# Kernel tuning notes

Hardware: AMD Instinct MI355X
Metric: run time of the kernel (lower is better)

The kernel has to match this reference:

```python
import jax, jax.numpy as jnp
import numpy as np

D_MODEL = 1024
NUM_HEADS = 16
D_FF = 4096
BATCH = 4
SEQ = 1024
EPS = 1e-5
ROPE_THETA = 10000.0


def trunc_normal(key, shape):
    # approximate torch trunc_normal_(mean=0, std=1, a=-2, b=2)
    return jax.random.truncated_normal(key, -2.0, 2.0, shape, dtype=jnp.float32)


def setup_inputs() -> dict:
    key = jax.random.key(0)
    ks = jax.random.split(key, 10)
    d, h, f = D_MODEL, NUM_HEADS, D_FF
    return {
        "x": jax.random.normal(ks[0], (BATCH, SEQ, d), dtype=jnp.float32),
        "wq": trunc_normal(ks[1], (d, d)),
        "wk": trunc_normal(ks[2], (d, d)),
        "wv": trunc_normal(ks[3], (d, d)),
        "wo": trunc_normal(ks[4], (d, d)),
        "w1": trunc_normal(ks[5], (f, d)),
        "w2": trunc_normal(ks[6], (d, f)),
        "w3": trunc_normal(ks[7], (f, d)),
        "g1": trunc_normal(ks[8], (d,)),
        "g2": trunc_normal(ks[9], (d,)),
    }


def rms_norm(x, g):
    # source sums (x^2 + eps) then divides by d -> mean(x^2) + eps
    rms = jnp.sqrt(jnp.mean(jnp.square(x), axis=-1, keepdims=True) + EPS)
    return x * g / rms


def apply_rope(x, pos):
    # x: [b, h, s, d_k]; interleaved-pair rotation, theta=ROPE_THETA
    dk = x.shape[-1]
    inv_freq = ROPE_THETA ** (-jnp.arange(0, dk, 2, dtype=jnp.float32) / dk)
    ang = pos[:, None].astype(jnp.float32) * inv_freq[None, :]  # [s, dk/2]
    cos, sin = jnp.cos(ang), jnp.sin(ang)
    x1, x2 = x[..., 0::2], x[..., 1::2]
    r1 = x1 * cos - x2 * sin
    r2 = x1 * sin + x2 * cos
    return jnp.stack([r1, r2], axis=-1).reshape(x.shape)


def reference(x, wq, wk, wv, wo, w1, w2, w3, g1, g2):
    b, s, d = x.shape
    h, dk = NUM_HEADS, d // NUM_HEADS
    pos = jnp.arange(s)

    # --- attention sub-block (pre-norm) ---
    y = rms_norm(x, g1)
    q = (y @ wq.T).reshape(b, s, h, dk).transpose(0, 2, 1, 3)
    k = (y @ wk.T).reshape(b, s, h, dk).transpose(0, 2, 1, 3)
    v = (y @ wv.T).reshape(b, s, h, dk).transpose(0, 2, 1, 3)
    q = apply_rope(q, pos)
    k = apply_rope(k, pos)
    scores = jnp.einsum('bhqd,bhkd->bhqk', q, k) / jnp.sqrt(jnp.float32(dk))
    causal = jnp.tril(jnp.ones((s, s), dtype=bool))
    scores = jnp.where(causal, scores, -jnp.inf)
    attn = jax.nn.softmax(scores, axis=-1)
    ctx = jnp.einsum('bhqk,bhkd->bhqd', attn, v)
    ctx = ctx.transpose(0, 2, 1, 3).reshape(b, s, d)
    x = x + ctx @ wo.T

    # --- SwiGLU FFN sub-block (pre-norm) ---
    y = rms_norm(x, g2)
    l1 = y @ w1.T
    glu = (jax.nn.sigmoid(l1) * l1) * (y @ w3.T)
    return x + glu @ w2.T
```

## Files before the change

kernel.cpp:

```cpp
#include <hip/hip_runtime.h>

typedef __bf16 bf16;
typedef __attribute__((ext_vector_type(8))) __bf16 bf16x8;
typedef __attribute__((ext_vector_type(4))) float f32x4;

static __device__ __forceinline__ int swz4(int r) { return (r >> 1) & 3; }

static __device__ __forceinline__ void async_cp16(void* lds, const void* g) {
  __builtin_amdgcn_global_load_lds((__attribute__((address_space(1))) void*)g,
                                   (__attribute__((address_space(3))) void*)lds,
                                   16, 0, 0);
}

static __device__ __forceinline__ f32x4 mfma16(bf16x8 a, bf16x8 b, f32x4 c) {
  return __builtin_amdgcn_mfma_f32_16x16x32_bf16(a, b, c, 0, 0, 0);
}

static __device__ __forceinline__ unsigned short bfbits(float f) {
  bf16 b = (bf16)f;
  return __builtin_bit_cast(unsigned short, b);
}

extern "C" __global__ void prep_kernel(
    const float* __restrict__ wq, const float* __restrict__ wk,
    const float* __restrict__ wv, const float* __restrict__ wo,
    const float* __restrict__ w1, const float* __restrict__ w3,
    const float* __restrict__ w2,
    unsigned short* __restrict__ WQH, unsigned short* __restrict__ WQL,
    unsigned short* __restrict__ WKH, unsigned short* __restrict__ WKL,
    unsigned short* __restrict__ WVH, unsigned short* __restrict__ WOH,
    unsigned short* __restrict__ W1H, unsigned short* __restrict__ W3H,
    unsigned short* __restrict__ W2H, float2* __restrict__ rope) {
  const int seg = blockIdx.y;
  const int i = blockIdx.x * 256 + threadIdx.x;
  if (seg == 7) {
    if (i >= 32768) return;
    int s = i >> 5, fi = i & 31;
    float inv_freq = powf(10000.0f, -(2.0f * (float)fi) / 64.0f);
    float ang = (float)s * inv_freq;
    float2 cs;
    cs.x = cosf(ang);
    cs.y = sinf(ang);
    rope[i] = cs;
    return;
  }
  const float* src;
  unsigned short* hi_;
  unsigned short* lo_ = nullptr;
  int n4;
  switch (seg) {
    case 0: src = wq; hi_ = WQH; lo_ = WQL; n4 = 262144; break;
    case 1: src = wk; hi_ = WKH; lo_ = WKL; n4 = 262144; break;
    case 2: src = wv; hi_ = WVH; n4 = 262144; break;
    case 3: src = wo; hi_ = WOH; n4 = 262144; break;
    case 4: src = w1; hi_ = W1H; n4 = 1048576; break;
    case 5: src = w3; hi_ = W3H; n4 = 1048576; break;
    default: src = w2; hi_ = W2H; n4 = 1048576; break;
  }
  if (i >= n4) return;
  float4 v = ((const float4*)src)[i];
  bf16 b0 = (bf16)v.x, b1 = (bf16)v.y, b2 = (bf16)v.z, b3 = (bf16)v.w;
  ushort4 oh;
  oh.x = __builtin_bit_cast(unsigned short, b0);
  oh.y = __builtin_bit_cast(unsigned short, b1);
  oh.z = __builtin_bit_cast(unsigned short, b2);
  oh.w = __builtin_bit_cast(unsigned short, b3);
  ((ushort4*)hi_)[i] = oh;
  if (lo_) {
    ushort4 ol;
    ol.x = bfbits(v.x - (float)b0);
    ol.y = bfbits(v.y - (float)b1);
    ol.z = bfbits(v.z - (float)b2);
    ol.w = bfbits(v.w - (float)b3);
    ((ushort4*)lo_)[i] = ol;
  }
}

extern "C" __global__ __launch_bounds__(256) void rmsnorm_kernel(
    const float* __restrict__ x, const float* __restrict__ g,
    unsigned short* __restrict__ yhi, unsigned short* __restrict__ ylo) {
  int row = blockIdx.x;
  int t = threadIdx.x;
  const float4 xv = *(const float4*)(x + (size_t)row * 1024 + t * 4);
  float ss = xv.x * xv.x + xv.y * xv.y + xv.z * xv.z + xv.w * xv.w;
#pragma unroll
  for (int d = 1; d < 64; d <<= 1) ss += __shfl_xor(ss, d, 64);
  __shared__ float red[4];
  if ((t & 63) == 0) red[t >> 6] = ss;
  __syncthreads();
  float tot = red[0] + red[1] + red[2] + red[3];
  float inv = 1.0f / sqrtf(tot * (1.0f / 1024.0f) + 1e-5f);
  const float4 gv = *(const float4*)(g + t * 4);
  float y0 = xv.x * gv.x * inv, y1 = xv.y * gv.y * inv;
  float y2 = xv.z * gv.z * inv, y3 = xv.w * gv.w * inv;
  bf16 b0 = (bf16)y0, b1 = (bf16)y1, b2 = (bf16)y2, b3 = (bf16)y3;
  ushort4 oh;
  oh.x = __builtin_bit_cast(unsigned short, b0);
  oh.y = __builtin_bit_cast(unsigned short, b1);
  oh.z = __builtin_bit_cast(unsigned short, b2);
  oh.w = __builtin_bit_cast(unsigned short, b3);
  ((ushort4*)yhi)[(size_t)row * 256 + t] = oh;
  if (ylo) {
    ushort4 ol;
    ol.x = bfbits(y0 - (float)b0);
    ol.y = bfbits(y1 - (float)b1);
    ol.z = bfbits(y2 - (float)b2);
    ol.w = bfbits(y3 - (float)b3);
    ((ushort4*)ylo)[(size_t)row * 256 + t] = ol;
  }
}

template <int EPI>
__global__ __launch_bounds__(256, 2) void gemm_nt(
    const bf16* __restrict__ A, const bf16* __restrict__ B, int N, int K, int ldk,
    float* __restrict__ outF, bf16* __restrict__ outB,
    const float* __restrict__ resF) {
  const int bid = blockIdx.x;
  const int xcd = bid & 7, sq = bid >> 3;
  const int z = sq >> 5;
  const int rem = sq & 31;
  const size_t tm = (size_t)(xcd * 4 + (rem >> 3)) * 128;
  const size_t tn = (size_t)(rem & 7) * 128;
  A += (size_t)z * K;
  B += (size_t)z * K;
  __shared__ alignas(16) bf16 As[128 * 32];
  __shared__ alignas(16) bf16 Bs[128 * 32];
  const int tid = threadIdx.x;
  const int lane = tid & 63, wave = tid >> 6;
  const int lo = lane & 15, hi = lane >> 4;
  const int wm = wave >> 1, wn = wave & 1;
  f32x4 acc[4][4] = {};
  for (int k0 = 0; k0 < K; k0 += 32) {
    __syncthreads();
#pragma unroll
    for (int i2 = 0; i2 < 2; i2++) {
      int p = tid + 256 * i2;
      int row = p >> 2, kcp = p & 3;
      int kcl = kcp ^ swz4(row);
      async_cp16((char*)As + (size_t)p * 16, A + (tm + row) * (size_t)ldk + k0 + kcl * 8);
      async_cp16((char*)Bs + (size_t)p * 16, B + (tn + row) * (size_t)ldk + k0 + kcl * 8);
    }
    __syncthreads();
    bf16x8 fa[4], fb[4];
#pragma unroll
    for (int i = 0; i < 4; i++) {
      int ra = wm * 64 + i * 16 + lo;
      fa[i] = *(const bf16x8*)((const char*)As + ra * 64 + ((hi ^ swz4(ra)) << 4));
      int rb = wn * 64 + i * 16 + lo;
      fb[i] = *(const bf16x8*)((const char*)Bs + rb * 64 + ((hi ^ swz4(rb)) << 4));
    }
    __builtin_amdgcn_s_setprio(1);
#pragma unroll
    for (int i = 0; i < 4; i++)
#pragma unroll
      for (int j = 0; j < 4; j++) acc[i][j] = mfma16(fa[i], fb[j], acc[i][j]);
    __builtin_amdgcn_s_setprio(0);
  }
#pragma unroll
  for (int i = 0; i < 4; i++)
#pragma unroll
    for (int j = 0; j < 4; j++)
#pragma unroll
      for (int r = 0; r < 4; r++) {
        size_t m = tm + wm * 64 + i * 16 + hi * 4 + r;
        size_t n = tn + wn * 64 + j * 16 + lo;
        float v = acc[i][j][r];
        if constexpr (EPI == 0) {
          size_t idx = (((m >> 10) * 16 + (n >> 6)) * 64 + (n & 63)) * 1024 + (m & 1023);
          outB[idx] = (bf16)v;
        } else if constexpr (EPI == 1) {
          size_t idx = m * (size_t)N + n;
          outF[idx] = v + resF[idx];
        } else {
          atomicAdd(&outF[m * (size_t)N + n], v);
        }
      }
}

extern "C" __global__ __launch_bounds__(512, 2) void gemm_up_kernel(
    const bf16* __restrict__ A, const bf16* __restrict__ B1,
    const bf16* __restrict__ B3, bf16* __restrict__ G) {
  __shared__ alignas(16) bf16 LA[2][2][256][32];
  __shared__ alignas(16) bf16 LB1[2][2][128][32];
  __shared__ alignas(16) bf16 LB3[2][2][128][32];
  const int tid = threadIdx.x;
  const int lane = tid & 63, wave = tid >> 6;
  const int lo = lane & 15, hi = lane >> 4;
  const int wm = wave >> 1, wn = wave & 1;
  const int bid = blockIdx.x;
  const int xcd = bid & 7, sq = bid >> 3;
  const size_t tn = (size_t)(xcd * 4 + (sq & 3)) * 128;
  const size_t tm = (size_t)(sq >> 2) * 256;

  f32x4 acc1[4][4] = {}, acc3[4][4] = {};

  auto stageA = [&](int kt, int kh, int buf) {
#pragma unroll
    for (int i2 = 0; i2 < 2; i2++) {
      int s = i2 * 512 + tid;
      int r = s >> 2, c = s & 3;
      async_cp16((char*)&LA[buf][kh][0][0] + (size_t)s * 16,
                 A + (tm + r) * (size_t)1024 + kt * 64 + kh * 32 + ((c ^ swz4(r)) << 3));
    }
  };
  auto stageB = [&](const bf16* __restrict__ Bsrc, bf16* dstBase, int kt, int kh) {
    int r = tid >> 2, c = tid & 3;
    async_cp16((char*)dstBase + (size_t)tid * 16,
               Bsrc + (tn + r) * (size_t)1024 + kt * 64 + kh * 32 + ((c ^ swz4(r)) << 3));
  };

  stageA(0, 0, 0);
  stageB(B1, &LB1[0][0][0][0], 0, 0);
  stageB(B3, &LB3[0][0][0][0], 0, 0);
  stageA(0, 1, 0);
  stageB(B1, &LB1[0][1][0][0], 0, 1);
  stageB(B3, &LB3[0][1][0][0], 0, 1);
  stageA(1, 0, 1);
  stageB(B1, &LB1[1][0][0][0], 1, 0);
  stageB(B3, &LB3[1][0][0][0], 1, 0);
  asm volatile("s_waitcnt vmcnt(4)");
  __builtin_amdgcn_s_barrier();

  for (int t = 0; t < 16; t++) {
    const int p = t & 1;
    bf16x8 fa[4], fb[4];
#pragma unroll
    for (int i = 0; i < 4; i++) {
      int ra = wm * 64 + i * 16 + lo;
      fa[i] = *(const bf16x8*)&LA[p][0][ra][(hi ^ swz4(ra)) << 3];
      int rb = wn * 64 + i * 16 + lo;
      fb[i] = *(const bf16x8*)&LB1[p][0][rb][(hi ^ swz4(rb)) << 3];
    }
    if (t + 1 < 16) stageA(t + 1, 1, p ^ 1);
    __builtin_amdgcn_s_barrier();
    asm volatile("s_waitcnt lgkmcnt(0)");
    __builtin_amdgcn_sched_barrier(0);
    __builtin_amdgcn_s_setprio(1);
#pragma unroll
    for (int i = 0; i < 4; i++)
#pragma unroll
      for (int j = 0; j < 4; j++) acc1[i][j] = mfma16(fa[i], fb[j], acc1[i][j]);
    __builtin_amdgcn_s_setprio(0);
    __builtin_amdgcn_s_barrier();
#pragma unroll
    for (int i = 0; i < 4; i++) {
      int rb = wn * 64 + i * 16 + lo;
      fb[i] = *(const bf16x8*)&LB3[p][0][rb][(hi ^ swz4(rb)) << 3];
    }
    if (t + 1 < 16) {
      stageB(B1, &LB1[p ^ 1][1][0][0], t + 1, 1);
      stageB(B3, &LB3[p ^ 1][1][0][0], t + 1, 1);
    }
    __builtin_amdgcn_s_barrier();
    asm volatile("s_waitcnt lgkmcnt(0)");
    __builtin_amdgcn_sched_barrier(0);
    __builtin_amdgcn_s_setprio(1);
#pragma unroll
    for (int i = 0; i < 4; i++)
#pragma unroll
      for (int j = 0; j < 4; j++) acc3[i][j] = mfma16(fa[i], fb[j], acc3[i][j]);
    __builtin_amdgcn_s_setprio(0);
    __builtin_amdgcn_s_barrier();
#pragma unroll
    for (int i = 0; i < 4; i++) {
      int ra = wm * 64 + i * 16 + lo;
      fa[i] = *(const bf16x8*)&LA[p][1][ra][(hi ^ swz4(ra)) << 3];
      int rb = wn * 64 + i * 16 + lo;
      fb[i] = *(const bf16x8*)&LB1[p][1][rb][(hi ^ swz4(rb)) << 3];
    }
    if (t + 2 < 16) stageA(t + 2, 0, p);
    __builtin_amdgcn_s_barrier();
    asm volatile("s_waitcnt lgkmcnt(0)");
    __builtin_amdgcn_sched_barrier(0);
    __builtin_amdgcn_s_setprio(1);
#pragma unroll
    for (int i = 0; i < 4; i++)
#pragma unroll
      for (int j = 0; j < 4; j++) acc1[i][j] = mfma16(fa[i], fb[j], acc1[i][j]);
    __builtin_amdgcn_s_setprio(0);
    __builtin_amdgcn_s_barrier();
#pragma unroll
    for (int i = 0; i < 4; i++) {
      int rb = wn * 64 + i * 16 + lo;
      fb[i] = *(const bf16x8*)&LB3[p][1][rb][(hi ^ swz4(rb)) << 3];
    }
    if (t + 2 < 16) {
      stageB(B1, &LB1[p][0][0][0], t + 2, 0);
      stageB(B3, &LB3[p][0][0][0], t + 2, 0);
    }
    __builtin_amdgcn_s_barrier();
    asm volatile("s_waitcnt lgkmcnt(0)");
    __builtin_amdgcn_sched_barrier(0);
    __builtin_amdgcn_s_setprio(1);
#pragma unroll
    for (int i = 0; i < 4; i++)
#pragma unroll
      for (int j = 0; j < 4; j++) acc3[i][j] = mfma16(fa[i], fb[j], acc3[i][j]);
    __builtin_amdgcn_s_setprio(0);
    if (t + 2 < 16) {
      asm volatile("s_waitcnt vmcnt(4)");
    } else if (t + 1 < 16) {
      asm volatile("s_waitcnt vmcnt(0)");
    }
    __builtin_amdgcn_s_barrier();
  }

#pragma unroll
  for (int i = 0; i < 4; i++)
#pragma unroll
    for (int j = 0; j < 4; j++)
#pragma unroll
      for (int r = 0; r < 4; r++) {
        size_t m = tm + wm * 64 + i * 16 + hi * 4 + r;
        size_t n = tn + wn * 64 + j * 16 + lo;
        float v1 = acc1[i][j][r], v3 = acc3[i][j][r];
        G[m * 4096 + n] = (bf16)(v1 / (1.0f + __expf(-v1)) * v3);
      }
}

extern "C" __global__ __launch_bounds__(256, 2) void gemm_qk_kernel(
    const bf16* __restrict__ Ah, const bf16* __restrict__ Al,
    const bf16* __restrict__ BhQ, const bf16* __restrict__ BlQ,
    const bf16* __restrict__ BhK, const bf16* __restrict__ BlK,
    const float2* __restrict__ rope,
    bf16* __restrict__ OhQ, bf16* __restrict__ OlQ,
    bf16* __restrict__ OhK, bf16* __restrict__ OlK) {
  const int bid = blockIdx.x;
  const int xcd = bid & 7, sq = bid >> 3;
  const int zqk = sq >> 5;
  const int rem = sq & 31;
  const size_t tm = (size_t)(xcd * 4 + (rem >> 3)) * 128;
  const size_t tn = (size_t)(rem & 7) * 128;
  const bf16* Bh = zqk ? BhK : BhQ;
  const bf16* Bl = zqk ? BlK : BlQ;
  bf16* Oh = zqk ? OhK : OhQ;
  bf16* Ol = zqk ? OlK : OlQ;
  __shared__ alignas(16) bf16 Ahs[128 * 32], Als[128 * 32], Bhs[128 * 32], Bls[128 * 32];
  const int tid = threadIdx.x;
  const int lane = tid & 63, wave = tid >> 6;
  const int lo = lane & 15, hi = lane >> 4;
  const int wm = wave >> 1, wn = wave & 1;
  const int K = 1024;
  f32x4 acc[4][4] = {};
  for (int k0 = 0; k0 < K; k0 += 32) {
    __syncthreads();
#pragma unroll
    for (int i2 = 0; i2 < 2; i2++) {
      int p = tid + 256 * i2;
      int row = p >> 2;
      int kcl = (p & 3) ^ swz4(row);
      size_t ga = (tm + row) * (size_t)K + k0 + kcl * 8;
      size_t gb = (tn + row) * (size_t)K + k0 + kcl * 8;
      async_cp16((char*)Ahs + (size_t)p * 16, Ah + ga);
      async_cp16((char*)Als + (size_t)p * 16, Al + ga);
      async_cp16((char*)Bhs + (size_t)p * 16, Bh + gb);
      async_cp16((char*)Bls + (size_t)p * 16, Bl + gb);
    }
    __syncthreads();
    bf16x8 fah[4], fal[4], fbh[4], fbl[4];
#pragma unroll
    for (int i = 0; i < 4; i++) {
      int ra = wm * 64 + i * 16 + lo;
      int oa = ra * 64 + ((hi ^ swz4(ra)) << 4);
      fah[i] = *(const bf16x8*)((const char*)Ahs + oa);
      fal[i] = *(const bf16x8*)((const char*)Als + oa);
      int rb = wn * 64 + i * 16 + lo;
      int ob = rb * 64 + ((hi ^ swz4(rb)) << 4);
      fbh[i] = *(const bf16x8*)((const char*)Bhs + ob);
      fbl[i] = *(const bf16x8*)((const char*)Bls + ob);
    }
    __builtin_amdgcn_s_setprio(1);
#pragma unroll
    for (int i = 0; i < 4; i++)
#pragma unroll
      for (int j = 0; j < 4; j++) {
        f32x4 a = acc[i][j];
        a = mfma16(fah[i], fbh[j], a);
        a = mfma16(fah[i], fbl[j], a);
        a = mfma16(fal[i], fbh[j], a);
        acc[i][j] = a;
      }
    __builtin_amdgcn_s_setprio(0);
  }
#pragma unroll
  for (int i = 0; i < 4; i++)
#pragma unroll
    for (int j = 0; j < 4; j++)
#pragma unroll
      for (int r = 0; r < 4; r++) {
        float v = acc[i][j][r];
        float vp = __shfl_xor(v, 1, 64);
        size_t m = tm + wm * 64 + i * 16 + hi * 4 + r;
        size_t n = tn + wn * 64 + j * 16 + lo;
        int s = (int)(m & 1023);
        int pi = (int)((n & 63) >> 1);
        float2 cs = rope[s * 32 + pi];
        float res = (n & 1) ? (vp * cs.y + v * cs.x) : (v * cs.x - vp * cs.y);
        size_t idx = (((m >> 10) * 16 + (n >> 6)) * 1024 + (m & 1023)) * 64 + (n & 63);
        bf16 hb = (bf16)res;
        Oh[idx] = hb;
        Ol[idx] = (bf16)(res - (float)hb);
      }
}

extern "C" __global__ __launch_bounds__(256, 4) void flash_kernel(
    const bf16* __restrict__ qhi, const bf16* __restrict__ qlo,
    const bf16* __restrict__ khi, const bf16* __restrict__ klo,
    const bf16* __restrict__ vT, bf16* __restrict__ ctx) {
  const int bid = blockIdx.x;
  const int qb = bid >> 6;
  const int bh = bid & 63;
  const int tid = threadIdx.x;
  const int wave = tid >> 6, lane = tid & 63;
  const int lo = lane & 15, hi = lane >> 4;

  __shared__ alignas(16) bf16 Ksh[2][64][32];
  __shared__ alignas(16) bf16 Ksl[2][64][32];
  __shared__ alignas(16) bf16 Vs[2][64][32];
  __shared__ alignas(16) bf16 P[4][16][72];

  size_t qoff = ((size_t)bh * 1024 + qb * 64 + wave * 16 + lo) * 64;
  bf16x8 qh[2], ql[2];
#pragma unroll
  for (int ks = 0; ks < 2; ks++) {
    qh[ks] = *(const bf16x8*)(qhi + qoff + ks * 32 + hi * 8);
    ql[ks] = *(const bf16x8*)(qlo + qoff + ks * 32 + hi * 8);
  }

  const int srow = tid >> 2;
  const int scl = (tid & 3) ^ swz4(srow);
  const size_t kgb = (size_t)bh * 1024 * 64;
  const size_t vgb = ((size_t)bh * 64 + srow) * 1024;

  float mrun[4] = {-1e30f, -1e30f, -1e30f, -1e30f};
  float lrun[4] = {0.f, 0.f, 0.f, 0.f};
  f32x4 o[4] = {};
  const float scale = 0.125f;

  for (int kt = 0; kt <= qb; kt++) {
    __syncthreads();
#pragma unroll
    for (int i = 0; i < 2; i++) {
      int p = tid + 256 * i;
      size_t gk = kgb + (size_t)(kt * 64 + srow) * 64 + i * 32 + scl * 8;
      async_cp16((char*)Ksh + (size_t)p * 16, khi + gk);
      async_cp16((char*)Ksl + (size_t)p * 16, klo + gk);
      async_cp16((char*)Vs + (size_t)p * 16, vT + vgb + kt * 64 + i * 32 + scl * 8);
    }
    __syncthreads();

    f32x4 sv[4];
    __builtin_amdgcn_s_setprio(1);
#pragma unroll
    for (int nb = 0; nb < 4; nb++) {
      f32x4 a = {0.f, 0.f, 0.f, 0.f};
#pragma unroll
      for (int ks = 0; ks < 2; ks++) {
        int row = nb * 16 + lo;
        int off16 = (ks * 64 + row) * 4 + (hi ^ swz4(row));
        bf16x8 kh = *(const bf16x8*)((const char*)Ksh + off16 * 16);
        bf16x8 kl = *(const bf16x8*)((const char*)Ksl + off16 * 16);
        a = mfma16(qh[ks], kh, a);
        a = mfma16(qh[ks], kl, a);
        a = mfma16(ql[ks], kh, a);
      }
      sv[nb] = a;
    }
    __builtin_amdgcn_s_setprio(0);

    const bool mt = (kt == qb);
#pragma unroll
    for (int nb = 0; nb < 4; nb++)
#pragma unroll
      for (int r = 0; r < 4; r++) {
        float s = sv[nb][r] * scale;
        if (mt) {
          int kp = nb * 16 + lo;
          int qr = wave * 16 + hi * 4 + r;
          if (kp > qr) s = -1e30f;
        }
        sv[nb][r] = s;
      }
    float mnew[4], rs[4];
#pragma unroll
    for (int r = 0; r < 4; r++) {
      float mx = fmaxf(fmaxf(sv[0][r], sv[1][r]), fmaxf(sv[2][r], sv[3][r]));
#pragma unroll
      for (int d = 1; d < 16; d <<= 1) mx = fmaxf(mx, __shfl_xor(mx, d, 64));
      mnew[r] = fmaxf(mrun[r], mx);
      float sc = __expf(mrun[r] - mnew[r]);
      lrun[r] *= sc;
#pragma unroll
      for (int db = 0; db < 4; db++) o[db][r] *= sc;
      mrun[r] = mnew[r];
      rs[r] = 0.f;
    }
#pragma unroll
    for (int nb = 0; nb < 4; nb++)
#pragma unroll
      for (int r = 0; r < 4; r++) {
        float p = __expf(sv[nb][r] - mnew[r]);
        bf16 pb = (bf16)p;
        rs[r] += (float)pb;
        P[wave][hi * 4 + r][nb * 16 + lo] = pb;
      }
#pragma unroll
    for (int r = 0; r < 4; r++) {
      float t = rs[r];
#pragma unroll
      for (int d = 1; d < 16; d <<= 1) t += __shfl_xor(t, d, 64);
      lrun[r] += t;
    }
    bf16x8 pa[2];
#pragma unroll
    for (int ks = 0; ks < 2; ks++) pa[ks] = *(const bf16x8*)&P[wave][lo][ks * 32 + hi * 8];
    __builtin_amdgcn_s_setprio(1);
#pragma unroll
    for (int db = 0; db < 4; db++)
#pragma unroll
      for (int ks = 0; ks < 2; ks++) {
        int row = db * 16 + lo;
        int off16 = (ks * 64 + row) * 4 + (hi ^ swz4(row));
        bf16x8 vf = *(const bf16x8*)((const char*)Vs + off16 * 16);
        o[db] = mfma16(pa[ks], vf, o[db]);
      }
    __builtin_amdgcn_s_setprio(0);
  }
  int b = bh >> 4, h = bh & 15;
#pragma unroll
  for (int db = 0; db < 4; db++)
#pragma unroll
    for (int r = 0; r < 4; r++) {
      float val = o[db][r] / lrun[r];
      size_t row = (size_t)b * 1024 + qb * 64 + wave * 16 + hi * 4 + r;
      ctx[row * 1024 + h * 64 + db * 16 + lo] = (bf16)val;
    }
}


extern "C" void kernel_launch(void* const* d_in, const int* in_sizes, int n_in,
                              void* d_out, int out_size, void* d_ws, size_t ws_size,
                              hipStream_t stream) {
  (void)in_sizes; (void)n_in; (void)out_size; (void)ws_size;
  const float* x  = (const float*)d_in[0];
  const float* wq = (const float*)d_in[1];
  const float* wk = (const float*)d_in[2];
  const float* wv = (const float*)d_in[3];
  const float* wo = (const float*)d_in[4];
  const float* w1 = (const float*)d_in[5];
  const float* w2 = (const float*)d_in[6];
  const float* w3 = (const float*)d_in[7];
  const float* g1 = (const float*)d_in[8];
  const float* g2 = (const float*)d_in[9];
  float* out = (float*)d_out;

  char* ws = (char*)d_ws;
  size_t off = 0;
  auto alloc = [&](size_t bytes) {
    char* p = ws + off;
    off += (bytes + 255) & ~(size_t)255;
    return p;
  };
  const size_t MB2 = 1024u * 1024u * 2u;
  const size_t MB8 = 4096u * 1024u * 2u;
  void* WQH = alloc(MB2);  void* WQL = alloc(MB2);
  void* WKH = alloc(MB2);  void* WKL = alloc(MB2);
  void* WVH = alloc(MB2);  void* WOH = alloc(MB2);
  void* W1H = alloc(MB8);  void* W3H = alloc(MB8);  void* W2H = alloc(MB8);
  void* ROPE = alloc(32768u * 8u);
  void* Y1H = alloc(MB8);  void* Y1L = alloc(MB8);
  void* QH = alloc(MB8);   void* QL = alloc(MB8);
  void* KH = alloc(MB8);   void* KL = alloc(MB8);
  void* VT = alloc(MB8);
  void* CTX = alloc(MB8);
  void* Y2H = alloc(MB8);
  void* GLU = QH;

  prep_kernel<<<dim3(4096, 8), dim3(256), 0, stream>>>(
      wq, wk, wv, wo, w1, w3, w2,
      (unsigned short*)WQH, (unsigned short*)WQL, (unsigned short*)WKH,
      (unsigned short*)WKL, (unsigned short*)WVH, (unsigned short*)WOH,
      (unsigned short*)W1H, (unsigned short*)W3H, (unsigned short*)W2H,
      (float2*)ROPE);

  rmsnorm_kernel<<<dim3(4096), dim3(256), 0, stream>>>(
      x, g1, (unsigned short*)Y1H, (unsigned short*)Y1L);

  gemm_qk_kernel<<<dim3(512), dim3(256), 0, stream>>>(
      (const bf16*)Y1H, (const bf16*)Y1L,
      (const bf16*)WQH, (const bf16*)WQL, (const bf16*)WKH, (const bf16*)WKL,
      (const float2*)ROPE,
      (bf16*)QH, (bf16*)QL, (bf16*)KH, (bf16*)KL);

  gemm_nt<0><<<dim3(256), dim3(256), 0, stream>>>(
      (const bf16*)Y1H, (const bf16*)WVH, 1024, 1024, 1024,
      nullptr, (bf16*)VT, nullptr);

  flash_kernel<<<dim3(1024), dim3(256), 0, stream>>>(
      (const bf16*)QH, (const bf16*)QL, (const bf16*)KH, (const bf16*)KL,
      (const bf16*)VT, (bf16*)CTX);

  gemm_nt<1><<<dim3(256), dim3(256), 0, stream>>>(
      (const bf16*)CTX, (const bf16*)WOH, 1024, 1024, 1024,
      out, nullptr, x);

  rmsnorm_kernel<<<dim3(4096), dim3(256), 0, stream>>>(
      out, g2, (unsigned short*)Y2H, nullptr);

  gemm_up_kernel<<<dim3(512), dim3(512), 0, stream>>>(
      (const bf16*)Y2H, (const bf16*)W1H, (const bf16*)W3H, (bf16*)GLU);

  gemm_nt<5><<<dim3(1024), dim3(256), 0, stream>>>(
      (const bf16*)GLU, (const bf16*)W2H, 1024, 1024, 4096,
      out, nullptr, nullptr);
}
```

Baseline: 330.6 us.

## Streamline gemm_up main loop with fewer barriers and precomputed addresses

```diff
diff --git a/kernel.cpp b/kernel.cpp
--- a/kernel.cpp
+++ b/kernel.cpp
@@ -194,115 +194,91 @@
 
   f32x4 acc1[4][4] = {}, acc3[4][4] = {};
 
-  auto stageA = [&](int kt, int kh, int buf) {
-#pragma unroll
-    for (int i2 = 0; i2 < 2; i2++) {
-      int s = i2 * 512 + tid;
-      int r = s >> 2, c = s & 3;
-      async_cp16((char*)&LA[buf][kh][0][0] + (size_t)s * 16,
-                 A + (tm + r) * (size_t)1024 + kt * 64 + kh * 32 + ((c ^ swz4(r)) << 3));
-    }
+  int offA[4], offB[4];
+#pragma unroll
+  for (int i = 0; i < 4; i++) {
+    int ra = wm * 64 + i * 16 + lo;
+    offA[i] = ra * 64 + ((hi ^ swz4(ra)) << 4);
+    int rb = wn * 64 + i * 16 + lo;
+    offB[i] = rb * 64 + ((hi ^ swz4(rb)) << 4);
+  }
+
+  const int r0 = tid >> 2, c0 = tid & 3;
+  const bf16* pA0 = A + (tm + r0) * (size_t)1024 + ((c0 ^ swz4(r0)) << 3);
+  const bf16* pB1 = B1 + (tn + r0) * (size_t)1024 + ((c0 ^ swz4(r0)) << 3);
+  const bf16* pB3 = B3 + (tn + r0) * (size_t)1024 + ((c0 ^ swz4(r0)) << 3);
+
+  auto stA = [&](char* plane) {
+    async_cp16(plane + tid * 16, pA0);
+    async_cp16(plane + (512 + tid) * 16, pA0 + 128 * 1024);
+    pA0 += 32;
   };
-  auto stageB = [&](const bf16* __restrict__ Bsrc, bf16* dstBase, int kt, int kh) {
-    int r = tid >> 2, c = tid & 3;
-    async_cp16((char*)dstBase + (size_t)tid * 16,
-               Bsrc + (tn + r) * (size_t)1024 + kt * 64 + kh * 32 + ((c ^ swz4(r)) << 3));
+  auto stB = [&](char* plane1, char* plane3) {
+    async_cp16(plane1 + tid * 16, pB1);
+    pB1 += 32;
+    async_cp16(plane3 + tid * 16, pB3);
+    pB3 += 32;
   };
 
-  stageA(0, 0, 0);
-  stageB(B1, &LB1[0][0][0][0], 0, 0);
-  stageB(B3, &LB3[0][0][0][0], 0, 0);
-  stageA(0, 1, 0);
-  stageB(B1, &LB1[0][1][0][0], 0, 1);
-  stageB(B3, &LB3[0][1][0][0], 0, 1);
-  stageA(1, 0, 1);
-  stageB(B1, &LB1[1][0][0][0], 1, 0);
-  stageB(B3, &LB3[1][0][0][0], 1, 0);
+  stA((char*)&LA[0][0][0][0]); stB((char*)&LB1[0][0][0][0], (char*)&LB3[0][0][0][0]);
+  stA((char*)&LA[0][1][0][0]); stB((char*)&LB1[0][1][0][0], (char*)&LB3[0][1][0][0]);
+  stA((char*)&LA[1][0][0][0]); stB((char*)&LB1[1][0][0][0], (char*)&LB3[1][0][0][0]);
   asm volatile("s_waitcnt vmcnt(4)");
   __builtin_amdgcn_s_barrier();
 
-  for (int t = 0; t < 16; t++) {
-    const int p = t & 1;
-    bf16x8 fa[4], fb[4];
-#pragma unroll
-    for (int i = 0; i < 4; i++) {
-      int ra = wm * 64 + i * 16 + lo;
-      fa[i] = *(const bf16x8*)&LA[p][0][ra][(hi ^ swz4(ra)) << 3];
-      int rb = wn * 64 + i * 16 + lo;
-      fb[i] = *(const bf16x8*)&LB1[p][0][rb][(hi ^ swz4(rb)) << 3];
-    }
-    if (t + 1 < 16) stageA(t + 1, 1, p ^ 1);
-    __builtin_amdgcn_s_barrier();
-    asm volatile("s_waitcnt lgkmcnt(0)");
-    __builtin_amdgcn_sched_barrier(0);
-    __builtin_amdgcn_s_setprio(1);
-#pragma unroll
-    for (int i = 0; i < 4; i++)
-#pragma unroll
-      for (int j = 0; j < 4; j++) acc1[i][j] = mfma16(fa[i], fb[j], acc1[i][j]);
-    __builtin_amdgcn_s_setprio(0);
-    __builtin_amdgcn_s_barrier();
-#pragma unroll
-    for (int i = 0; i < 4; i++) {
-      int rb = wn * 64 + i * 16 + lo;
-      fb[i] = *(const bf16x8*)&LB3[p][0][rb][(hi ^ swz4(rb)) << 3];
-    }
-    if (t + 1 < 16) {
-      stageB(B1, &LB1[p ^ 1][1][0][0], t + 1, 1);
-      stageB(B3, &LB3[p ^ 1][1][0][0], t + 1, 1);
-    }
-    __builtin_amdgcn_s_barrier();
-    asm volatile("s_waitcnt lgkmcnt(0)");
-    __builtin_amdgcn_sched_barrier(0);
-    __builtin_amdgcn_s_setprio(1);
-#pragma unroll
-    for (int i = 0; i < 4; i++)
-#pragma unroll
-      for (int j = 0; j < 4; j++) acc3[i][j] = mfma16(fa[i], fb[j], acc3[i][j]);
-    __builtin_amdgcn_s_setprio(0);
-    __builtin_amdgcn_s_barrier();
-#pragma unroll
-    for (int i = 0; i < 4; i++) {
-      int ra = wm * 64 + i * 16 + lo;
-      fa[i] = *(const bf16x8*)&LA[p][1][ra][(hi ^ swz4(ra)) << 3];
-      int rb = wn * 64 + i * 16 + lo;
-      fb[i] = *(const bf16x8*)&LB1[p][1][rb][(hi ^ swz4(rb)) << 3];
-    }
-    if (t + 2 < 16) stageA(t + 2, 0, p);
-    __builtin_amdgcn_s_barrier();
-    asm volatile("s_waitcnt lgkmcnt(0)");
-    __builtin_amdgcn_sched_barrier(0);
-    __builtin_amdgcn_s_setprio(1);
-#pragma unroll
-    for (int i = 0; i < 4; i++)
-#pragma unroll
-      for (int j = 0; j < 4; j++) acc1[i][j] = mfma16(fa[i], fb[j], acc1[i][j]);
-    __builtin_amdgcn_s_setprio(0);
-    __builtin_amdgcn_s_barrier();
-#pragma unroll
-    for (int i = 0; i < 4; i++) {
-      int rb = wn * 64 + i * 16 + lo;
-      fb[i] = *(const bf16x8*)&LB3[p][1][rb][(hi ^ swz4(rb)) << 3];
-    }
-    if (t + 2 < 16) {
-      stageB(B1, &LB1[p][0][0][0], t + 2, 0);
-      stageB(B3, &LB3[p][0][0][0], t + 2, 0);
-    }
-    __builtin_amdgcn_s_barrier();
-    asm volatile("s_waitcnt lgkmcnt(0)");
-    __builtin_amdgcn_sched_barrier(0);
-    __builtin_amdgcn_s_setprio(1);
-#pragma unroll
-    for (int i = 0; i < 4; i++)
-#pragma unroll
-      for (int j = 0; j < 4; j++) acc3[i][j] = mfma16(fa[i], fb[j], acc3[i][j]);
-    __builtin_amdgcn_s_setprio(0);
-    if (t + 2 < 16) {
-      asm volatile("s_waitcnt vmcnt(4)");
-    } else if (t + 1 < 16) {
-      asm volatile("s_waitcnt vmcnt(0)");
-    }
-    __builtin_amdgcn_s_barrier();
+#define UP_RD(ARR, P, KH, OFF) \
+  (*(const bf16x8*)((const char*)&ARR[P][KH][0][0] + (OFF)))
+
+#define UP_MFMA(ACC)                                        \
+  __builtin_amdgcn_s_setprio(1);                            \
+  _Pragma("unroll") for (int i = 0; i < 4; i++)             \
+    _Pragma("unroll") for (int j = 0; j < 4; j++)           \
+      ACC[i][j] = mfma16(fa[i], fb[j], ACC[i][j]);          \
+  __builtin_amdgcn_s_setprio(0);
+
+#define UP_TILE(T, P)                                                          \
+  {                                                                            \
+    bf16x8 fa[4], fb[4];                                                       \
+                                     \
+    _Pragma("unroll") for (int i = 0; i < 4; i++) {                            \
+      fa[i] = UP_RD(LA, P, 0, offA[i]);                                        \
+      fb[i] = UP_RD(LB1, P, 0, offB[i]);                                       \
+    }                                                                          \
+    if ((T) + 1 < 16) stA((char*)&LA[(P) ^ 1][1][0][0]);                       \
+    UP_MFMA(acc1)                                                              \
+    __builtin_amdgcn_s_barrier();                                              \
+                                     \
+    _Pragma("unroll") for (int j = 0; j < 4; j++)                              \
+      fb[j] = UP_RD(LB3, P, 0, offB[j]);                                       \
+    if ((T) + 1 < 16)                                                          \
+      stB((char*)&LB1[(P) ^ 1][1][0][0], (char*)&LB3[(P) ^ 1][1][0][0]);       \
+    UP_MFMA(acc3)                                                              \
+    __builtin_amdgcn_s_barrier();                                              \
+                                     \
+    _Pragma("unroll") for (int i = 0; i < 4; i++) {                            \
+      fa[i] = UP_RD(LA, P, 1, offA[i]);                                        \
+      fb[i] = UP_RD(LB1, P, 1, offB[i]);                                       \
+    }                                                                          \
+    if ((T) + 2 < 16) stA((char*)&LA[P][0][0][0]);                             \
+    UP_MFMA(acc1)                                                              \
+    __builtin_amdgcn_s_barrier();                                              \
+                         \
+    _Pragma("unroll") for (int j = 0; j < 4; j++)                              \
+      fb[j] = UP_RD(LB3, P, 1, offB[j]);                                       \
+    if ((T) + 2 < 16)                                                          \
+      stB((char*)&LB1[P][0][0][0], (char*)&LB3[P][0][0][0]);                   \
+    UP_MFMA(acc3)                                                              \
+    if ((T) + 2 < 16) {                                                        \
+      asm volatile("s_waitcnt vmcnt(4)");                                      \
+    } else if ((T) + 1 < 16) {                                                 \
+      asm volatile("s_waitcnt vmcnt(0)");                                      \
+    }                                                                          \
+    __builtin_amdgcn_s_barrier();                                              \
+  }
+
+  for (int tt = 0; tt < 16; tt += 2) {
+    UP_TILE(tt, 0)
+    UP_TILE(tt + 1, 1)
   }
 
 #pragma unroll
```

Measured after the change: 330.5 us. Within noise of the previous version (-0.0%).
